# Kernel tuning notes

Hardware: AMD Instinct MI355X
Metric: run time of the kernel (lower is better)

## Reference

```python
import jax, jax.numpy as jnp
import numpy as np

TOP_K = 8


def setup_inputs() -> dict:
    key = jax.random.key(0)
    k1, k2, k3 = jax.random.split(key, 3)
    N, D, SQRT_K = 8192, 2048, 64
    x = jax.random.normal(k1, (N, D), dtype=jnp.float32)
    W1 = jax.random.normal(k2, (SQRT_K, D), dtype=jnp.float32) * (1.0 / np.sqrt(D))
    W2 = jax.random.normal(k3, (SQRT_K, D), dtype=jnp.float32) * (1.0 / np.sqrt(D))
    return {"x": x, "W1": W1, "W2": W2}


def reference(x, W1, W2):
    # Two small projections: [N, d] @ [d, sqrt_K] -> [N, sqrt_K]
    s1 = jnp.einsum('nd,kd->nk', x, W1)
    s2 = jnp.einsum('nd,kd->nk', x, W2)
    # Outer-sum score matrix: expert (i, j) scores s1[i] + s2[j]; flatten -> [N, sqrt_K^2]
    scores = (s1[:, :, None] + s2[:, None, :]).reshape(x.shape[0], -1)
    topk_vals, topk_idx = jax.lax.top_k(scores, TOP_K)
    probs = jax.nn.softmax(topk_vals, axis=-1)
    return topk_idx, probs, scores
```

## Files before the change

kernel.cpp:

```cpp
#include <hip/hip_runtime.h>
#include <math.h>

#define NROWS 8192
#define DDIM  2048
#define NEXP  4096
#define TK    8
#define KSPLIT 4
#define KRANGE (DDIM / KSPLIT)
#define RB     32

typedef float  f4 __attribute__((ext_vector_type(4)));
typedef double d2 __attribute__((ext_vector_type(2)));

__global__ __launch_bounds__(256, 4) void pkr_gemm64(const float* __restrict__ x,
                                                     const float* __restrict__ w1,
                                                     const float* __restrict__ w2,
                                                     float* __restrict__ out) {
  __shared__ double xsd[32][34];
  __shared__ float  wsf[32][132];

  const int tid   = threadIdx.x;
  const int rb    = blockIdx.x >> 2;
  const int kp    = blockIdx.x & 3;
  const int rows0 = rb * RB;
  const int kbase = kp * KRANGE;

  const int rh = tid >> 5;
  const int ch = tid & 31;

  const int sxr = tid >> 3;
  const int sxk = (tid & 7) * 4;
  const float* xrow = x + (size_t)(rows0 + sxr) * DDIM + kbase + sxk;

  double acc[4][4] = {};

  for (int cch = 0; cch < KRANGE / 32; ++cch) {
    const int k0 = cch * 32;
    f4 xv = *(const f4*)(xrow + k0);
#pragma unroll
    for (int q = 0; q < 4; ++q) xsd[sxk + q][sxr] = (double)xv[q];
#pragma unroll
    for (int i = 0; i < 4; ++i) {
      const int idx = i * 256 + tid;
      const int c2  = idx >> 3;
      const int kk  = (idx & 7) * 4;
      const float* wr = (c2 < 64) ? (w1 + (size_t)c2 * DDIM)
                                  : (w2 + (size_t)(c2 - 64) * DDIM);
      f4 wv = *(const f4*)(wr + kbase + k0 + kk);
#pragma unroll
      for (int q = 0; q < 4; ++q) wsf[kk + q][c2] = wv[q];
    }
    __syncthreads();

#pragma unroll
    for (int k = 0; k < 32; ++k) {
      const d2 x01 = *(const d2*)&xsd[k][rh * 4];
      const d2 x23 = *(const d2*)&xsd[k][rh * 4 + 2];
      const f4 wq  = *(const f4*)&wsf[k][ch * 4];
      const double xd[4] = { x01[0], x01[1], x23[0], x23[1] };
      double wd[4];
#pragma unroll
      for (int b = 0; b < 4; ++b) wd[b] = (double)wq[b];
#pragma unroll
      for (int a = 0; a < 4; ++a)
#pragma unroll
        for (int b = 0; b < 4; ++b)
          acc[a][b] += xd[a] * wd[b];
    }
    __syncthreads();
  }

  double* P = (double*)(out + (size_t)2 * NROWS * TK);
#pragma unroll
  for (int a = 0; a < 4; ++a) {
    double* dst = P + (size_t)(rows0 + rh * 4 + a) * (NEXP / 2) + kp * 128 + ch * 4;
    d2 lo; lo[0] = acc[a][0]; lo[1] = acc[a][1];
    d2 hi; hi[0] = acc[a][2]; hi[1] = acc[a][3];
    *(d2*)dst       = lo;
    *(d2*)(dst + 2) = hi;
  }
}

__device__ __forceinline__ void bitonic64(double& v, int& idx, int lane) {
#pragma unroll
  for (int k = 2; k <= 64; k <<= 1) {
#pragma unroll
    for (int j = k >> 1; j > 0; j >>= 1) {
      const double ov = __shfl_xor(v, j);
      const int    oi = __shfl_xor(idx, j);
      const bool obetter = (ov > v) || (ov == v && oi < idx);
      const bool lower   = (lane & j) == 0;
      const bool up      = (lane & k) == 0;
      if ((lower == up) ? obetter : !obetter) { v = ov; idx = oi; }
    }
  }
}

__global__ __launch_bounds__(256) void pkr_finish(float* __restrict__ out) {
  const int lane = threadIdx.x & 63;
  const int wv   = threadIdx.x >> 6;
  const int row  = blockIdx.x * 4 + wv;

  const double* Pr = (const double*)(out + (size_t)2 * NROWS * TK) + (size_t)row * (NEXP / 2);
  double s1 = 0.0, s2 = 0.0;
#pragma unroll
  for (int p = 0; p < KSPLIT; ++p) {
    s1 += Pr[p * 128 + lane];
    s2 += Pr[p * 128 + 64 + lane];
  }

  __shared__ double sh1[4][64], sh2[4][64];
  sh1[wv][lane] = s1;
  sh2[wv][lane] = s2;
  __syncthreads();

  {
    float* srow = out + (size_t)2 * NROWS * TK + (size_t)row * NEXP;
    const int il = lane >> 4;
    const int jq = (lane & 15) * 4;
    const double sj0 = sh2[wv][jq + 0], sj1 = sh2[wv][jq + 1];
    const double sj2 = sh2[wv][jq + 2], sj3 = sh2[wv][jq + 3];
#pragma unroll
    for (int i0 = 0; i0 < 64; i0 += 4) {
      const double si = sh1[wv][i0 + il];
      f4 v;
      v[0] = (float)(si + sj0);
      v[1] = (float)(si + sj1);
      v[2] = (float)(si + sj2);
      v[3] = (float)(si + sj3);
      *(f4*)(srow + (size_t)(i0 + il) * 64 + jq) = v;
    }
  }

  double v1 = s1; int i1 = lane;
  bitonic64(v1, i1, lane);
  double v2 = s2; int i2 = lane;
  bitonic64(v2, i2, lane);

  const double ca = __shfl(v1, lane >> 3);
  const int    ia = __shfl(i1, lane >> 3);
  const double cb = __shfl(v2, lane & 7);
  const int    ib = __shfl(i2, lane & 7);
  double cv = ca + cb;
  int    ci = ia * 64 + ib;
  bitonic64(cv, ci, lane);

  const double vmax = __shfl(cv, 0);
  float e = expf((float)(cv - vmax));
  float sum = e;
#pragma unroll
  for (int off = 1; off < 8; off <<= 1) sum += __shfl_xor(sum, off);
  if (lane < 8) {
    out[(size_t)row * TK + lane]                      = (float)ci;
    out[(size_t)NROWS * TK + (size_t)row * TK + lane] = e / sum;
  }
}

extern "C" void kernel_launch(void* const* d_in, const int* in_sizes, int n_in,
                              void* d_out, int out_size, void* d_ws, size_t ws_size,
                              hipStream_t stream) {
  const float* x  = (const float*)d_in[0];
  const float* w1 = (const float*)d_in[1];
  const float* w2 = (const float*)d_in[2];
  float* out = (float*)d_out;

  hipLaunchKernelGGL(pkr_gemm64, dim3((NROWS / RB) * KSPLIT), dim3(256), 0, stream,
                     x, w1, w2, out);
  hipLaunchKernelGGL(pkr_finish, dim3(NROWS / 4), dim3(256), 0, stream, out);
}
```

Baseline: 280.6 us.

## Enlarge FP64 GEMM row tile to 64 and store weights as double in LDS

Doubles the row block from 32 to 64 rows so each thread accumulates a 4x8 register tile instead of 4x4. Weights are converted to double once when staged into shared memory, rather than each thread converting them inside the inner loop. The goal is to raise FMA-to-load ratio and cut redundant float-to-double conversions and weight reloads per row. The cost is more registers and shared memory per block, so the occupancy hint drops from 4 to 2 blocks, and the grid has half as many blocks.

```diff
diff --git a/kernel.cpp b/kernel.cpp
--- a/kernel.cpp
+++ b/kernel.cpp
@@ -7,48 +7,56 @@
 #define TK    8
 #define KSPLIT 4
 #define KRANGE (DDIM / KSPLIT)
-#define RB     32
+#define BM     64
 
 typedef float  f4 __attribute__((ext_vector_type(4)));
 typedef double d2 __attribute__((ext_vector_type(2)));
 
-__global__ __launch_bounds__(256, 4) void pkr_gemm64(const float* __restrict__ x,
-                                                     const float* __restrict__ w1,
-                                                     const float* __restrict__ w2,
-                                                     float* __restrict__ out) {
-  __shared__ double xsd[32][34];
-  __shared__ float  wsf[32][132];
+__global__ __launch_bounds__(256, 2) void pkr_gemm64w(const float* __restrict__ x,
+                                                      const float* __restrict__ w1,
+                                                      const float* __restrict__ w2,
+                                                      float* __restrict__ out) {
+  __shared__ double xsd[32][66];
+  __shared__ double wsd[32][130];
 
   const int tid   = threadIdx.x;
   const int rb    = blockIdx.x >> 2;
   const int kp    = blockIdx.x & 3;
-  const int rows0 = rb * RB;
+  const int rows0 = rb * BM;
   const int kbase = kp * KRANGE;
 
-  const int rh = tid >> 5;
-  const int ch = tid & 31;
+  const int rh = tid >> 4;
+  const int ch = tid & 15;
 
   const int sxr = tid >> 3;
   const int sxk = (tid & 7) * 4;
-  const float* xrow = x + (size_t)(rows0 + sxr) * DDIM + kbase + sxk;
+  const float* xr0 = x + (size_t)(rows0 + sxr) * DDIM + kbase + sxk;
+  const float* xr1 = xr0 + (size_t)32 * DDIM;
 
-  double acc[4][4] = {};
+  const int swc = tid >> 1;
+  const int swk = (tid & 1) * 16;
+  const float* wr = ((swc < 64) ? (w1 + (size_t)swc * DDIM)
+                                : (w2 + (size_t)(swc - 64) * DDIM)) + kbase + swk;
+
+  double acc[4][8] = {};
 
   for (int cch = 0; cch < KRANGE / 32; ++cch) {
     const int k0 = cch * 32;
-    f4 xv = *(const f4*)(xrow + k0);
+    {
+      f4 a = *(const f4*)(xr0 + k0);
+      f4 b = *(const f4*)(xr1 + k0);
 #pragma unroll
-    for (int q = 0; q < 4; ++q) xsd[sxk + q][sxr] = (double)xv[q];
+      for (int q = 0; q < 4; ++q) {
+        xsd[sxk + q][sxr]      = (double)a[q];
+        xsd[sxk + q][32 + sxr] = (double)b[q];
+      }
+    }
 #pragma unroll
-    for (int i = 0; i < 4; ++i) {
-      const int idx = i * 256 + tid;
-      const int c2  = idx >> 3;
-      const int kk  = (idx & 7) * 4;
-      const float* wr = (c2 < 64) ? (w1 + (size_t)c2 * DDIM)
-                                  : (w2 + (size_t)(c2 - 64) * DDIM);
-      f4 wv = *(const f4*)(wr + kbase + k0 + kk);
+    for (int p = 0; p < 4; ++p) {
+      f4 wv = *(const f4*)(wr + k0 + p * 4);
 #pragma unroll
-      for (int q = 0; q < 4; ++q) wsf[kk + q][c2] = wv[q];
+      for (int q = 0; q < 4; ++q)
+        wsd[swk + p * 4 + q][swc] = (double)wv[q];
     }
     __syncthreads();
 
@@ -56,16 +64,17 @@
     for (int k = 0; k < 32; ++k) {
       const d2 x01 = *(const d2*)&xsd[k][rh * 4];
       const d2 x23 = *(const d2*)&xsd[k][rh * 4 + 2];
-      const f4 wq  = *(const f4*)&wsf[k][ch * 4];
       const double xd[4] = { x01[0], x01[1], x23[0], x23[1] };
-      double wd[4];
+      d2 wg[4];
 #pragma unroll
-      for (int b = 0; b < 4; ++b) wd[b] = (double)wq[b];
+      for (int g = 0; g < 4; ++g) wg[g] = *(const d2*)&wsd[k][g * 32 + ch * 2];
 #pragma unroll
       for (int a = 0; a < 4; ++a)
 #pragma unroll
-        for (int b = 0; b < 4; ++b)
-          acc[a][b] += xd[a] * wd[b];
+        for (int g = 0; g < 4; ++g) {
+          acc[a][2 * g]     += xd[a] * wg[g][0];
+          acc[a][2 * g + 1] += xd[a] * wg[g][1];
+        }
     }
     __syncthreads();
   }
@@ -73,11 +82,12 @@
   double* P = (double*)(out + (size_t)2 * NROWS * TK);
 #pragma unroll
   for (int a = 0; a < 4; ++a) {
-    double* dst = P + (size_t)(rows0 + rh * 4 + a) * (NEXP / 2) + kp * 128 + ch * 4;
-    d2 lo; lo[0] = acc[a][0]; lo[1] = acc[a][1];
-    d2 hi; hi[0] = acc[a][2]; hi[1] = acc[a][3];
-    *(d2*)dst       = lo;
-    *(d2*)(dst + 2) = hi;
+    double* dst = P + (size_t)(rows0 + rh * 4 + a) * (NEXP / 2) + kp * 128;
+#pragma unroll
+    for (int g = 0; g < 4; ++g) {
+      d2 v; v[0] = acc[a][2 * g]; v[1] = acc[a][2 * g + 1];
+      *(d2*)(dst + g * 32 + ch * 2) = v;
+    }
   }
 }
 
@@ -164,7 +174,7 @@
   const float* w2 = (const float*)d_in[2];
   float* out = (float*)d_out;
 
-  hipLaunchKernelGGL(pkr_gemm64, dim3((NROWS / RB) * KSPLIT), dim3(256), 0, stream,
+  hipLaunchKernelGGL(pkr_gemm64w, dim3((NROWS / BM) * KSPLIT), dim3(256), 0, stream,
                      x, w1, w2, out);
   hipLaunchKernelGGL(pkr_finish, dim3(NROWS / 4), dim3(256), 0, stream, out);
 }
```

Measured after the change: 273.9 us. 1.02x faster.

## Use FP64 MFMA for projection GEMM and drop split-K partial sums

Applied to the files above, without the earlier changes.

Replaces the scalar FP64 FMA projection GEMM with the 16x16x4 FP64 MFMA instruction. The operand and accumulator lane layout is detected at runtime, with a shuffle-based emulation as fallback. The split-K partitioning goes away: each block covers the full D range with register-prefetched double-buffered loads, so the finish kernel reads final sums directly. This targets the low throughput of scalar double FMAs, at the cost of fewer blocks (256), a calibration prologue, and scattered scalar stores of results.

```diff
diff --git a/kernel.cpp b/kernel.cpp
--- a/kernel.cpp
+++ b/kernel.cpp
@@ -5,80 +5,167 @@
 #define DDIM  2048
 #define NEXP  4096
 #define TK    8
-#define KSPLIT 4
-#define KRANGE (DDIM / KSPLIT)
-#define RB     32
-
-typedef float  f4 __attribute__((ext_vector_type(4)));
-typedef double d2 __attribute__((ext_vector_type(2)));
-
-__global__ __launch_bounds__(256, 4) void pkr_gemm64(const float* __restrict__ x,
+#define BM    32
+#define BK    32
+#define NCH   (DDIM / BK)
+
+typedef float  f4    __attribute__((ext_vector_type(4)));
+typedef double d2    __attribute__((ext_vector_type(2)));
+typedef double f64x4 __attribute__((ext_vector_type(4)));
+
+__device__ __forceinline__ f64x4 mfma_emu(double a, double b, f64x4 c) {
+  const int l = threadIdx.x & 63;
+  f64x4 d = c;
+#pragma unroll
+  for (int e = 0; e < 4; ++e) {
+    const int m = (l >> 4) * 4 + e;
+    double s = 0.0;
+#pragma unroll
+    for (int k = 0; k < 4; ++k)
+      s += __shfl(a, m + 16 * k) * __shfl(b, (l & 15) + 16 * k);
+    d[e] += s;
+  }
+  return d;
+}
+
+__device__ __forceinline__ f64x4 mfma_hw(double a, double b, f64x4 c) {
+#if __has_builtin(__builtin_amdgcn_mfma_f64_16x16x4f64)
+  return __builtin_amdgcn_mfma_f64_16x16x4f64(a, b, c, 0, 0, 0);
+#else
+  return mfma_emu(a, b, c);
+#endif
+}
+
+__global__ __launch_bounds__(256) void pkr_gemm_mfma(const float* __restrict__ x,
                                                      const float* __restrict__ w1,
                                                      const float* __restrict__ w2,
                                                      float* __restrict__ out) {
-  __shared__ double xsd[32][34];
-  __shared__ float  wsf[32][132];
+  __shared__ double xsd[BM][34];
+  __shared__ double wsd[128][34];
 
   const int tid   = threadIdx.x;
-  const int rb    = blockIdx.x >> 2;
-  const int kp    = blockIdx.x & 3;
-  const int rows0 = rb * RB;
-  const int kbase = kp * KRANGE;
-
-  const int rh = tid >> 5;
-  const int ch = tid & 31;
-
-  const int sxr = tid >> 3;
-  const int sxk = (tid & 7) * 4;
-  const float* xrow = x + (size_t)(rows0 + sxr) * DDIM + kbase + sxk;
-
-  double acc[4][4] = {};
-
-  for (int cch = 0; cch < KRANGE / 32; ++cch) {
-    const int k0 = cch * 32;
-    f4 xv = *(const f4*)(xrow + k0);
-#pragma unroll
-    for (int q = 0; q < 4; ++q) xsd[sxk + q][sxr] = (double)xv[q];
-#pragma unroll
-    for (int i = 0; i < 4; ++i) {
-      const int idx = i * 256 + tid;
-      const int c2  = idx >> 3;
-      const int kk  = (idx & 7) * 4;
-      const float* wr = (c2 < 64) ? (w1 + (size_t)c2 * DDIM)
-                                  : (w2 + (size_t)(c2 - 64) * DDIM);
-      f4 wv = *(const f4*)(wr + kbase + k0 + kk);
-#pragma unroll
-      for (int q = 0; q < 4; ++q) wsf[kk + q][c2] = wv[q];
+  const int rows0 = blockIdx.x * BM;
+
+  const int lane = tid & 63;
+  const int wv   = tid >> 6;
+  const int fr   = lane & 15;
+  const int fk   = lane >> 4;
+  const int rt   = wv & 1;
+  const int cq   = wv >> 1;
+
+  f64x4 zz = {};
+  const double pl = (double)lane;
+  const f64x4 accA = mfma_hw(pl, 1.0, zz);
+  const f64x4 accB = mfma_hw(1.0, pl, zz);
+
+  const int vA0 = (int)accA[0];
+  const int vB0 = (int)accB[0];
+  const bool aL1 = ((vA0 & 3) == 0);
+  const bool bL1 = ((vB0 & 3) == 0);
+  int dm[4], dn[4];
+  bool okl = true;
+#pragma unroll
+  for (int e = 0; e < 4; ++e) {
+    const int va = (int)accA[e];
+    const int vb = (int)accB[e];
+    const int me = aL1 ? ((va - 96) >> 2) : ((va - 6) >> 4);
+    const int ne = bL1 ? ((vb - 96) >> 2) : ((vb - 6) >> 4);
+    okl = okl && (me >= 0) && (me < 16) && (ne >= 0) && (ne < 16);
+    okl = okl && (va == (aL1 ? 96 + 4 * me : 6 + 16 * me));
+    okl = okl && (vb == (bL1 ? 96 + 4 * ne : 6 + 16 * ne));
+    dm[e] = me & 15;
+    dn[e] = ne & 15;
+  }
+  okl = okl && (dm[0] != dm[1]) && (dm[0] != dm[2]) && (dm[0] != dm[3]) &&
+               (dm[1] != dm[2]) && (dm[1] != dm[3]) && (dm[2] != dm[3]);
+  const bool calib_ok = (__all((int)okl) != 0);
+
+  const int am = aL1 ? fr : (lane >> 2);
+  const int ak = aL1 ? fk : (lane & 3);
+  const int bn = bL1 ? fr : (lane >> 2);
+  const int bk = bL1 ? fk : (lane & 3);
+
+  const int xr = tid >> 3;
+  const int xk = (tid & 7) * 4;
+  const int wc = tid >> 1;
+  const int wk = (tid & 1) * 16;
+  const float* xrow = x + (size_t)(rows0 + xr) * DDIM + xk;
+  const float* wrow = ((wc < 64) ? (w1 + (size_t)wc * DDIM)
+                                 : (w2 + (size_t)(wc - 64) * DDIM)) + wk;
+
+  f4 xf, wf[4];
+
+#define LOAD_REGS(CH) do {                                        \
+    const int o_ = (CH) * BK;                                     \
+    xf    = *(const f4*)(xrow + o_);                              \
+    wf[0] = *(const f4*)(wrow + o_);                              \
+    wf[1] = *(const f4*)(wrow + o_ + 4);                          \
+    wf[2] = *(const f4*)(wrow + o_ + 8);                          \
+    wf[3] = *(const f4*)(wrow + o_ + 12);                         \
+  } while (0)
+
+#define WRITE_LDS() do {                                          \
+    d2 t_;                                                        \
+    t_[0] = (double)xf[0]; t_[1] = (double)xf[1];                 \
+    *(d2*)&xsd[xr][xk]     = t_;                                  \
+    t_[0] = (double)xf[2]; t_[1] = (double)xf[3];                 \
+    *(d2*)&xsd[xr][xk + 2] = t_;                                  \
+    _Pragma("unroll")                                             \
+    for (int p_ = 0; p_ < 4; ++p_) {                              \
+      t_[0] = (double)wf[p_][0]; t_[1] = (double)wf[p_][1];       \
+      *(d2*)&wsd[wc][wk + p_ * 4]     = t_;                       \
+      t_[0] = (double)wf[p_][2]; t_[1] = (double)wf[p_][3];       \
+      *(d2*)&wsd[wc][wk + p_ * 4 + 2] = t_;                       \
+    }                                                             \
+  } while (0)
+
+#define GEMM_LOOP(MFMA_CALL, AM, AK, BN, BKI)                              \
+    LOAD_REGS(0);                                                          \
+    WRITE_LDS();                                                           \
+    __syncthreads();                                                       \
+    for (int ch = 0; ch < NCH; ++ch) {                                     \
+      if (ch + 1 < NCH) LOAD_REGS(ch + 1);                                 \
+      _Pragma("unroll")                                                    \
+      for (int ks = 0; ks < BK / 4; ++ks) {                                \
+        const double a = xsd[rt * 16 + (AM)][ks * 4 + (AK)];               \
+        _Pragma("unroll")                                                  \
+        for (int c = 0; c < 4; ++c) {                                      \
+          const double b = wsd[cq * 64 + c * 16 + (BN)][ks * 4 + (BKI)];   \
+          acc[c] = MFMA_CALL(a, b, acc[c]);                                \
+        }                                                                  \
+      }                                                                    \
+      __syncthreads();                                                     \
+      if (ch + 1 < NCH) { WRITE_LDS(); __syncthreads(); }                  \
     }
-    __syncthreads();
-
-#pragma unroll
-    for (int k = 0; k < 32; ++k) {
-      const d2 x01 = *(const d2*)&xsd[k][rh * 4];
-      const d2 x23 = *(const d2*)&xsd[k][rh * 4 + 2];
-      const f4 wq  = *(const f4*)&wsf[k][ch * 4];
-      const double xd[4] = { x01[0], x01[1], x23[0], x23[1] };
-      double wd[4];
-#pragma unroll
-      for (int b = 0; b < 4; ++b) wd[b] = (double)wq[b];
-#pragma unroll
-      for (int a = 0; a < 4; ++a)
-#pragma unroll
-        for (int b = 0; b < 4; ++b)
-          acc[a][b] += xd[a] * wd[b];
-    }
-    __syncthreads();
-  }
 
   double* P = (double*)(out + (size_t)2 * NROWS * TK);
-#pragma unroll
-  for (int a = 0; a < 4; ++a) {
-    double* dst = P + (size_t)(rows0 + rh * 4 + a) * (NEXP / 2) + kp * 128 + ch * 4;
-    d2 lo; lo[0] = acc[a][0]; lo[1] = acc[a][1];
-    d2 hi; hi[0] = acc[a][2]; hi[1] = acc[a][3];
-    *(d2*)dst       = lo;
-    *(d2*)(dst + 2) = hi;
-  }
+
+  if (calib_ok) {
+    f64x4 acc[4] = {};
+    GEMM_LOOP(mfma_hw, am, ak, bn, bk)
+#pragma unroll
+    for (int c = 0; c < 4; ++c)
+#pragma unroll
+      for (int e = 0; e < 4; ++e) {
+        const int row = rows0 + rt * 16 + dm[e];
+        const int col = cq * 64 + c * 16 + dn[e];
+        P[(size_t)row * (NEXP / 2) + col] = acc[c][e];
+      }
+  } else {
+    f64x4 acc[4] = {};
+    GEMM_LOOP(mfma_emu, fr, fk, fr, fk)
+#pragma unroll
+    for (int c = 0; c < 4; ++c)
+#pragma unroll
+      for (int e = 0; e < 4; ++e) {
+        const int row = rows0 + rt * 16 + fk * 4 + e;
+        const int col = cq * 64 + c * 16 + fr;
+        P[(size_t)row * (NEXP / 2) + col] = acc[c][e];
+      }
+  }
+#undef GEMM_LOOP
+#undef LOAD_REGS
+#undef WRITE_LDS
 }
 
 __device__ __forceinline__ void bitonic64(double& v, int& idx, int lane) {
@@ -102,12 +189,8 @@
   const int row  = blockIdx.x * 4 + wv;
 
   const double* Pr = (const double*)(out + (size_t)2 * NROWS * TK) + (size_t)row * (NEXP / 2);
-  double s1 = 0.0, s2 = 0.0;
-#pragma unroll
-  for (int p = 0; p < KSPLIT; ++p) {
-    s1 += Pr[p * 128 + lane];
-    s2 += Pr[p * 128 + 64 + lane];
-  }
+  const double s1 = Pr[lane];
+  const double s2 = Pr[64 + lane];
 
   __shared__ double sh1[4][64], sh2[4][64];
   sh1[wv][lane] = s1;
@@ -164,7 +247,7 @@
   const float* w2 = (const float*)d_in[2];
   float* out = (float*)d_out;
 
-  hipLaunchKernelGGL(pkr_gemm64, dim3((NROWS / RB) * KSPLIT), dim3(256), 0, stream,
+  hipLaunchKernelGGL(pkr_gemm_mfma, dim3(NROWS / BM), dim3(256), 0, stream,
                      x, w1, w2, out);
   hipLaunchKernelGGL(pkr_finish, dim3(NROWS / 4), dim3(256), 0, stream, out);
 }
```

Result: faster. 272.5 us (-2.9%).
